# Optimization experiments

Hardware: AMD Instinct MI355X
Metric: run time of the kernel (lower is better)

## Reference

```python
import jax, jax.numpy as jnp
import numpy as np

GAMMA = 0.99  # init kwarg


def _discounted_returns(ep_rs):
    # reversed running_add = running_add*gamma + r, emitted per step
    def step(carry, r):
        carry = carry * GAMMA + r
        return carry, carry
    _, out = jax.lax.scan(step, jnp.float32(0.0), ep_rs, reverse=True)
    return out  # [T]


def setup_inputs() -> dict:
    key = jax.random.key(0)
    k1, k2, k3 = jax.random.split(key, 3)
    T, A = 2097152, 18
    weight = jax.random.normal(k1, (T, A), dtype=jnp.float32)
    ep_rs = jax.random.normal(k2, (T,), dtype=jnp.float32)
    ep_as = jax.random.randint(k3, (T,), 0, A, dtype=jnp.int64)
    return {"weight": weight, "ep_rs": ep_rs, "ep_as": ep_as}


def reference(weight, ep_rs, ep_as):
    d = _discounted_returns(ep_rs)
    d = d - jnp.mean(d)
    # cross_entropy with reduction='none': -log_softmax(weight)[t, ep_as[t]]
    logp = jax.nn.log_softmax(weight, axis=-1)  # [T, A]
    neg_log_prob = -jnp.take_along_axis(logp, ep_as[:, None], axis=-1)[:, 0]  # [T]
    return jnp.mean(neg_log_prob * d)
```

## Files before the change

### kernel.cpp

```cpp
#include <hip/hip_runtime.h>
#include <math.h>

#define T_TOTAL 2097152
#define A_DIM   18
#define GAMMA_D 0.99

#define CHUNK 256
#define NC    (T_TOTAL / CHUNK)
#define KTR   14

#define NB_MAIN 2048

__global__ void k_local(const float* __restrict__ r, double* __restrict__ L) {
    const int tid  = blockIdx.x * blockDim.x + threadIdx.x;
    const int c    = tid >> 6;
    const int lane = tid & 63;
    const float4 v = ((const float4*)r)[(size_t)c * 64 + lane];
    const double g = GAMMA_D;
    double w = pow(g, (double)(4 * lane)) *
               ((double)v.x + g * ((double)v.y + g * ((double)v.z + g * (double)v.w)));
    #pragma unroll
    for (int off = 32; off > 0; off >>= 1) w += __shfl_down(w, off, 64);
    if (lane == 0) L[c] = w;
}

__global__ void k_carry(const double* __restrict__ L, double* __restrict__ carry,
                        double G) {
    const int c = blockIdx.x * blockDim.x + threadIdx.x;
    double acc = 0.0, w = 1.0;
    #pragma unroll
    for (int m = 0; m < KTR; ++m) {
        int idx = c + 1 + m;
        if (idx < NC) acc += w * L[idx];
        w *= G;
    }
    carry[c] = acc;
}

__launch_bounds__(256)
__global__ void k_main(const float* __restrict__ wgt, const int* __restrict__ act,
                       const float* __restrict__ r, const double* __restrict__ carry,
                       double* __restrict__ partials) {
    __shared__ float  lds[CHUNK * A_DIM];
    __shared__ double ldsT[4];
    __shared__ double red[12];
    const int tid  = threadIdx.x;
    const int lane = tid & 63, wv = tid >> 6;
    const double g    = GAMMA_D;
    const double p    = pow(g, (double)tid);
    const double ip   = 1.0 / p;
    const double g256 = pow(g, 256.0);
    double s_d = 0.0, s_n = 0.0, s_nd = 0.0;

    for (int c = blockIdx.x; c < NC; c += gridDim.x) {
        __syncthreads();
        const float4* src = (const float4*)(wgt + (size_t)c * CHUNK * A_DIM);
        float4* dst = (float4*)lds;
        #pragma unroll
        for (int i = 0; i < 5; ++i) {
            int idx = tid + 256 * i;
            if (idx < CHUNK * A_DIM / 4) dst[idx] = src[idx];
        }
        const int row = c * CHUNK + tid;
        double ss = p * (double)r[row];
        #pragma unroll
        for (int off = 1; off < 64; off <<= 1) {
            double v = __shfl_down(ss, off, 64);
            ss += (lane + off < 64) ? v : 0.0;
        }
        if (lane == 0) ldsT[wv] = ss;
        __syncthreads();
        double tail = 0.0;
        #pragma unroll
        for (int m = 0; m < 4; ++m)
            if (m > wv) tail += ldsT[m];
        const double dval = ip * (ss + tail + g256 * carry[c]);
        const float* wr = lds + tid * A_DIM;
        float mx = wr[0];
        #pragma unroll
        for (int j = 1; j < A_DIM; ++j) mx = fmaxf(mx, wr[j]);
        float s = 0.0f;
        #pragma unroll
        for (int j = 0; j < A_DIM; ++j) s += expf(wr[j] - mx);
        const float nlp = mx + logf(s) - wr[act[row]];
        s_d  += dval;
        s_n  += (double)nlp;
        s_nd += (double)nlp * dval;
    }

    #pragma unroll
    for (int off = 32; off > 0; off >>= 1) {
        s_d  += __shfl_down(s_d,  off, 64);
        s_n  += __shfl_down(s_n,  off, 64);
        s_nd += __shfl_down(s_nd, off, 64);
    }
    if (lane == 0) { red[wv*3+0] = s_d; red[wv*3+1] = s_n; red[wv*3+2] = s_nd; }
    __syncthreads();
    if (tid == 0) {
        double a = 0.0, b = 0.0, cc = 0.0;
        #pragma unroll
        for (int i = 0; i < 4; ++i) { a += red[i*3]; b += red[i*3+1]; cc += red[i*3+2]; }
        partials[blockIdx.x*3+0] = a;
        partials[blockIdx.x*3+1] = b;
        partials[blockIdx.x*3+2] = cc;
    }
}

__global__ void k_final(const double* __restrict__ partials, float* __restrict__ out) {
    __shared__ double red[12];
    const int tid = threadIdx.x;
    double a = 0.0, b = 0.0, c = 0.0;
    for (int i = tid; i < NB_MAIN; i += 256) {
        a += partials[i*3+0];
        b += partials[i*3+1];
        c += partials[i*3+2];
    }
    #pragma unroll
    for (int off = 32; off > 0; off >>= 1) {
        a += __shfl_down(a, off, 64);
        b += __shfl_down(b, off, 64);
        c += __shfl_down(c, off, 64);
    }
    const int lane = tid & 63, wv = tid >> 6;
    if (lane == 0) { red[wv*3+0] = a; red[wv*3+1] = b; red[wv*3+2] = c; }
    __syncthreads();
    if (tid == 0) {
        double A_ = 0.0, B_ = 0.0, C_ = 0.0;
        #pragma unroll
        for (int i = 0; i < 4; ++i) { A_ += red[i*3]; B_ += red[i*3+1]; C_ += red[i*3+2]; }
        const double invT = 1.0 / (double)T_TOTAL;
        out[0] = (float)((C_ - (A_ * invT) * B_) * invT);
    }
}

extern "C" void kernel_launch(void* const* d_in, const int* in_sizes, int n_in,
                              void* d_out, int out_size, void* d_ws, size_t ws_size,
                              hipStream_t stream) {
    const float* weight = (const float*)d_in[0];
    const float* ep_rs  = (const float*)d_in[1];
    const int*   ep_as  = (const int*)  d_in[2];
    float* out = (float*)d_out;

    char* ws = (char*)d_ws;
    double* L        = (double*)(ws);
    double* carry    = (double*)(ws + (1 << 16));
    double* partials = (double*)(ws + (2 << 16));

    const double G = pow(GAMMA_D, (double)CHUNK);

    k_local <<<T_TOTAL / 4 / 256, 256, 0, stream>>>(ep_rs, L);
    k_carry <<<NC / 256,          256, 0, stream>>>(L, carry, G);
    k_main  <<<NB_MAIN,           256, 0, stream>>>(weight, ep_as, ep_rs, carry, partials);
    k_final <<<1,                 256, 0, stream>>>(partials, out);
}
```

Before: 234.2 us.

## Fuse chunk-sum and carry computation into main kernel with redundant per-block recompute

Removes the separate k_local and k_carry launches. Each block now handles four consecutive chunks and recomputes, for the 17 following chunks, the discounted chunk sums it needs from ep_rs. It then forms the truncated carries in LDS before the main log-softmax loop. This cuts two kernel launches and the global round-trip for L/carry. In exchange each block re-reads neighbouring reward chunks, adding redundant loads that should mostly hit in L2.

```diff
diff --git a/kernel.cpp b/kernel.cpp
--- a/kernel.cpp
+++ b/kernel.cpp
@@ -8,57 +8,55 @@
 #define CHUNK 256
 #define NC    (T_TOTAL / CHUNK)
 #define KTR   14
+#define CPB   4
+#define NB_MAIN (NC / CPB)
 
-#define NB_MAIN 2048
-
-__global__ void k_local(const float* __restrict__ r, double* __restrict__ L) {
-    const int tid  = blockIdx.x * blockDim.x + threadIdx.x;
-    const int c    = tid >> 6;
-    const int lane = tid & 63;
-    const float4 v = ((const float4*)r)[(size_t)c * 64 + lane];
-    const double g = GAMMA_D;
-    double w = pow(g, (double)(4 * lane)) *
-               ((double)v.x + g * ((double)v.y + g * ((double)v.z + g * (double)v.w)));
-    #pragma unroll
-    for (int off = 32; off > 0; off >>= 1) w += __shfl_down(w, off, 64);
-    if (lane == 0) L[c] = w;
-}
-
-__global__ void k_carry(const double* __restrict__ L, double* __restrict__ carry,
-                        double G) {
-    const int c = blockIdx.x * blockDim.x + threadIdx.x;
-    double acc = 0.0, w = 1.0;
-    #pragma unroll
-    for (int m = 0; m < KTR; ++m) {
-        int idx = c + 1 + m;
-        if (idx < NC) acc += w * L[idx];
-        w *= G;
-    }
-    carry[c] = acc;
-}
-
-__launch_bounds__(256)
-__global__ void k_main(const float* __restrict__ wgt, const int* __restrict__ act,
-                       const float* __restrict__ r, const double* __restrict__ carry,
-                       double* __restrict__ partials) {
+__global__ __launch_bounds__(256, 4)
+void k_mega(const float* __restrict__ wgt, const int* __restrict__ act,
+            const float* __restrict__ r, double* __restrict__ partials) {
     __shared__ float  lds[CHUNK * A_DIM];
+    __shared__ double ldsL[17];
+    __shared__ double ldsC[CPB];
     __shared__ double ldsT[4];
     __shared__ double red[12];
     const int tid  = threadIdx.x;
     const int lane = tid & 63, wv = tid >> 6;
+    const int c0   = CPB * blockIdx.x;
     const double g    = GAMMA_D;
+    const double G_   = pow(g, 256.0);
     const double p    = pow(g, (double)tid);
     const double ip   = 1.0 / p;
-    const double g256 = pow(g, 256.0);
+
+    const double w4 = pow(g, (double)(4 * lane));
+    for (int k = wv; k < 17; k += 4) {
+        const int cc = c0 + 1 + k;
+        double val = 0.0;
+        if (cc < NC) {
+            const float4 v = ((const float4*)r)[(size_t)cc * 64 + lane];
+            val = w4 * ((double)v.x + g * ((double)v.y + g * ((double)v.z + g * (double)v.w)));
+            #pragma unroll
+            for (int off = 32; off > 0; off >>= 1) val += __shfl_down(val, off, 64);
+        }
+        if (lane == 0) ldsL[k] = val;
+    }
+    __syncthreads();
+    if (tid < CPB) {
+        double acc = 0.0, wG = 1.0;
+        #pragma unroll
+        for (int m = 0; m < KTR; ++m) { acc += wG * ldsL[tid + m]; wG *= G_; }
+        ldsC[tid] = acc;
+    }
+
     double s_d = 0.0, s_n = 0.0, s_nd = 0.0;
 
-    for (int c = blockIdx.x; c < NC; c += gridDim.x) {
+    for (int i = 0; i < CPB; ++i) {
+        const int c = c0 + i;
         __syncthreads();
         const float4* src = (const float4*)(wgt + (size_t)c * CHUNK * A_DIM);
         float4* dst = (float4*)lds;
         #pragma unroll
-        for (int i = 0; i < 5; ++i) {
-            int idx = tid + 256 * i;
+        for (int q = 0; q < 5; ++q) {
+            int idx = tid + 256 * q;
             if (idx < CHUNK * A_DIM / 4) dst[idx] = src[idx];
         }
         const int row = c * CHUNK + tid;
@@ -74,7 +72,7 @@
         #pragma unroll
         for (int m = 0; m < 4; ++m)
             if (m > wv) tail += ldsT[m];
-        const double dval = ip * (ss + tail + g256 * carry[c]);
+        const double dval = ip * (ss + tail + G_ * ldsC[i]);
         const float* wr = lds + tid * A_DIM;
         float mx = wr[0];
         #pragma unroll
@@ -99,7 +97,7 @@
     if (tid == 0) {
         double a = 0.0, b = 0.0, cc = 0.0;
         #pragma unroll
-        for (int i = 0; i < 4; ++i) { a += red[i*3]; b += red[i*3+1]; cc += red[i*3+2]; }
+        for (int q = 0; q < 4; ++q) { a += red[q*3]; b += red[q*3+1]; cc += red[q*3+2]; }
         partials[blockIdx.x*3+0] = a;
         partials[blockIdx.x*3+1] = b;
         partials[blockIdx.x*3+2] = cc;
@@ -141,15 +139,8 @@
     const int*   ep_as  = (const int*)  d_in[2];
     float* out = (float*)d_out;
 
-    char* ws = (char*)d_ws;
-    double* L        = (double*)(ws);
-    double* carry    = (double*)(ws + (1 << 16));
-    double* partials = (double*)(ws + (2 << 16));
+    double* partials = (double*)d_ws;
 
-    const double G = pow(GAMMA_D, (double)CHUNK);
-
-    k_local <<<T_TOTAL / 4 / 256, 256, 0, stream>>>(ep_rs, L);
-    k_carry <<<NC / 256,          256, 0, stream>>>(L, carry, G);
-    k_main  <<<NB_MAIN,           256, 0, stream>>>(weight, ep_as, ep_rs, carry, partials);
-    k_final <<<1,                 256, 0, stream>>>(partials, out);
+    k_mega  <<<NB_MAIN, 256, 0, stream>>>(weight, ep_as, ep_rs, partials);
+    k_final <<<1,       256, 0, stream>>>(partials, out);
 }
```

Result: slower. 239.5 us (+2.3%).

## Materialize discounted returns in separate kernel and stream weights directly into registers

Applied to the files above, without the earlier changes.

Discounted returns are now computed in a dedicated kernel that fuses the carry computation and writes the full double-precision return array to workspace. The main kernel no longer stages weight rows through LDS or runs a per-chunk scan. Each thread instead loads two rows straight into registers, selects the chosen logit with a predicated loop, and runs in a single pass with no block barriers. This trades a 16MB extra global write and read of the returns for removing LDS traffic, syncs and scan work from the main loop, with twice as many blocks.

```diff
diff --git a/kernel.cpp b/kernel.cpp
--- a/kernel.cpp
+++ b/kernel.cpp
@@ -8,8 +8,7 @@
 #define CHUNK 256
 #define NC    (T_TOTAL / CHUNK)
 #define KTR   14
-
-#define NB_MAIN 2048
+#define NB_MAIN 4096
 
 __global__ void k_local(const float* __restrict__ r, double* __restrict__ L) {
     const int tid  = blockIdx.x * blockDim.x + threadIdx.x;
@@ -24,68 +23,90 @@
     if (lane == 0) L[c] = w;
 }
 
-__global__ void k_carry(const double* __restrict__ L, double* __restrict__ carry,
-                        double G) {
-    const int c = blockIdx.x * blockDim.x + threadIdx.x;
-    double acc = 0.0, w = 1.0;
+__global__ __launch_bounds__(256)
+void k_d(const float* __restrict__ r, const double* __restrict__ L,
+         double* __restrict__ d) {
+    const int tid = threadIdx.x, lane = tid & 63, wv = tid >> 6;
+    const int c = blockIdx.x * 4 + wv;
+    const double g  = GAMMA_D;
+    const double G_ = pow(g, 256.0);
+    double acc = 0.0, wG = 1.0;
     #pragma unroll
     for (int m = 0; m < KTR; ++m) {
-        int idx = c + 1 + m;
-        if (idx < NC) acc += w * L[idx];
-        w *= G;
+        const int idx = c + 1 + m;
+        if (idx < NC) acc += wG * L[idx];
+        wG *= G_;
     }
-    carry[c] = acc;
+    const float4 v = ((const float4*)r)[(size_t)c * 64 + lane];
+    const double u3 = (double)v.w;
+    const double u2 = (double)v.z + g * u3;
+    const double u1 = (double)v.y + g * u2;
+    const double u0 = (double)v.x + g * u1;
+    const double w4 = pow(g, (double)(4 * lane));
+    double S = w4 * u0;
+    #pragma unroll
+    for (int off = 1; off < 64; off <<= 1) {
+        const double t = __shfl_down(S, off, 64);
+        S += (lane + off < 64) ? t : 0.0;
+    }
+    double Snext = __shfl_down(S, 1, 64);
+    if (lane == 63) Snext = 0.0;
+    const double A  = (1.0 / w4) * (Snext + G_ * acc);
+    const double ig = 1.0 / g;
+    const double d0 = u0 + A;
+    const double d1 = u1 + ig * A;
+    const double d2 = u2 + (ig * ig) * A;
+    const double d3 = u3 + (ig * ig * ig) * A;
+    double2* dp = (double2*)(d + (size_t)c * CHUNK + 4 * lane);
+    dp[0] = make_double2(d0, d1);
+    dp[1] = make_double2(d2, d3);
 }
 
-__launch_bounds__(256)
-__global__ void k_main(const float* __restrict__ wgt, const int* __restrict__ act,
-                       const float* __restrict__ r, const double* __restrict__ carry,
-                       double* __restrict__ partials) {
-    __shared__ float  lds[CHUNK * A_DIM];
-    __shared__ double ldsT[4];
+__global__ __launch_bounds__(256, 4)
+void k_main(const float* __restrict__ wgt, const int* __restrict__ act,
+            const double* __restrict__ dret, double* __restrict__ partials) {
     __shared__ double red[12];
     const int tid  = threadIdx.x;
     const int lane = tid & 63, wv = tid >> 6;
-    const double g    = GAMMA_D;
-    const double p    = pow(g, (double)tid);
-    const double ip   = 1.0 / p;
-    const double g256 = pow(g, 256.0);
-    double s_d = 0.0, s_n = 0.0, s_nd = 0.0;
+    const size_t t0 = ((size_t)blockIdx.x * 256 + tid) * 2;
 
-    for (int c = blockIdx.x; c < NC; c += gridDim.x) {
-        __syncthreads();
-        const float4* src = (const float4*)(wgt + (size_t)c * CHUNK * A_DIM);
-        float4* dst = (float4*)lds;
+    const float4* wp = (const float4*)(wgt + t0 * A_DIM);
+    float w[36];
+    #pragma unroll
+    for (int q = 0; q < 9; ++q) {
+        const float4 v = wp[q];
+        w[4*q+0] = v.x; w[4*q+1] = v.y; w[4*q+2] = v.z; w[4*q+3] = v.w;
+    }
+    const int2    aa = *(const int2*)(act + t0);
+    const double2 dd = *(const double2*)(dret + t0);
+
+    double s_n = 0.0, s_nd = 0.0;
+    double s_d = dd.x + dd.y;
+    {
+        float mx = w[0];
         #pragma unroll
-        for (int i = 0; i < 5; ++i) {
-            int idx = tid + 256 * i;
-            if (idx < CHUNK * A_DIM / 4) dst[idx] = src[idx];
+        for (int j = 1; j < A_DIM; ++j) mx = fmaxf(mx, w[j]);
+        float s = 0.0f, wsel = 0.0f;
+        #pragma unroll
+        for (int j = 0; j < A_DIM; ++j) {
+            s += expf(w[j] - mx);
+            wsel = (j == aa.x) ? w[j] : wsel;
         }
-        const int row = c * CHUNK + tid;
-        double ss = p * (double)r[row];
+        const float nlp = mx + logf(s) - wsel;
+        s_n += (double)nlp;  s_nd += (double)nlp * dd.x;
+    }
+    {
+        float mx = w[18];
         #pragma unroll
-        for (int off = 1; off < 64; off <<= 1) {
-            double v = __shfl_down(ss, off, 64);
-            ss += (lane + off < 64) ? v : 0.0;
+        for (int j = 1; j < A_DIM; ++j) mx = fmaxf(mx, w[18 + j]);
+        float s = 0.0f, wsel = 0.0f;
+        #pragma unroll
+        for (int j = 0; j < A_DIM; ++j) {
+            s += expf(w[18 + j] - mx);
+            wsel = (j == aa.y) ? w[18 + j] : wsel;
         }
-        if (lane == 0) ldsT[wv] = ss;
-        __syncthreads();
-        double tail = 0.0;
-        #pragma unroll
-        for (int m = 0; m < 4; ++m)
-            if (m > wv) tail += ldsT[m];
-        const double dval = ip * (ss + tail + g256 * carry[c]);
-        const float* wr = lds + tid * A_DIM;
-        float mx = wr[0];
-        #pragma unroll
-        for (int j = 1; j < A_DIM; ++j) mx = fmaxf(mx, wr[j]);
-        float s = 0.0f;
-        #pragma unroll
-        for (int j = 0; j < A_DIM; ++j) s += expf(wr[j] - mx);
-        const float nlp = mx + logf(s) - wr[act[row]];
-        s_d  += dval;
-        s_n  += (double)nlp;
-        s_nd += (double)nlp * dval;
+        const float nlp = mx + logf(s) - wsel;
+        s_n += (double)nlp;  s_nd += (double)nlp * dd.y;
     }
 
     #pragma unroll
@@ -99,7 +120,7 @@
     if (tid == 0) {
         double a = 0.0, b = 0.0, cc = 0.0;
         #pragma unroll
-        for (int i = 0; i < 4; ++i) { a += red[i*3]; b += red[i*3+1]; cc += red[i*3+2]; }
+        for (int q = 0; q < 4; ++q) { a += red[q*3]; b += red[q*3+1]; cc += red[q*3+2]; }
         partials[blockIdx.x*3+0] = a;
         partials[blockIdx.x*3+1] = b;
         partials[blockIdx.x*3+2] = cc;
@@ -143,13 +164,11 @@
 
     char* ws = (char*)d_ws;
     double* L        = (double*)(ws);
-    double* carry    = (double*)(ws + (1 << 16));
-    double* partials = (double*)(ws + (2 << 16));
-
-    const double G = pow(GAMMA_D, (double)CHUNK);
+    double* dret     = (double*)(ws + (1 << 16));
+    double* partials = (double*)(ws + (1 << 16) + (16 << 20));
 
     k_local <<<T_TOTAL / 4 / 256, 256, 0, stream>>>(ep_rs, L);
-    k_carry <<<NC / 256,          256, 0, stream>>>(L, carry, G);
-    k_main  <<<NB_MAIN,           256, 0, stream>>>(weight, ep_as, ep_rs, carry, partials);
+    k_d     <<<NC / 4,            256, 0, stream>>>(ep_rs, L, dret);
+    k_main  <<<NB_MAIN,           256, 0, stream>>>(weight, ep_as, dret, partials);
     k_final <<<1,                 256, 0, stream>>>(partials, out);
 }
```

New measurement: 240.3 us. 1.03x slower.
